# Kernel tuning notes

Hardware: AMD Instinct MI355X
Metric: run time of the kernel (lower is better)

## Reference

```python
import jax, jax.numpy as jnp
import numpy as np

B, S, QD = 4, 2048, 1024
NH, KVH, DH = 16, 4, 64
WIN = 256  # sliding_window


def setup_inputs() -> dict:
    key = jax.random.key(0)
    ks = jax.random.split(key, 5)
    s = QD ** -0.5
    return {
        "hidden_states": jax.random.normal(ks[0], (B, S, QD), jnp.float32),
        "Wq": jax.random.normal(ks[1], (QD, NH * DH), jnp.float32) * s,
        "Wk": jax.random.normal(ks[2], (QD, KVH * DH), jnp.float32) * s,
        "Wv": jax.random.normal(ks[3], (QD, KVH * DH), jnp.float32) * s,
        "Wo": jax.random.normal(ks[4], (NH * DH, QD), jnp.float32) * s,
    }


def reference(hidden_states, Wq, Wk, Wv, Wo):
    x = hidden_states
    # QKV projections (torch Linear, no bias)
    q = (x @ Wq).reshape(B, S, NH, DH).transpose(0, 2, 1, 3)    # [B,NH,S,DH]
    k = (x @ Wk).reshape(B, S, KVH, DH).transpose(0, 2, 1, 3)   # [B,KVH,S,DH]
    v = (x @ Wv).reshape(B, S, KVH, DH).transpose(0, 2, 1, 3)
    # GQA: instead of repeat_interleave on k/v, group query heads per kv head
    g = NH // KVH
    qg = q.reshape(B, KVH, g, S, DH)
    scale = DH ** -0.5
    scores = jnp.einsum('bkgsd,bktd->bkgst', qg, k) * scale      # [B,KVH,g,S,S]
    # Sliding-window mask: torch SDPA treats a FLOAT mask as ADDITIVE, and the
    # original builds a 0/1 float mask (1 where |i-j| <= window). Faithful: add it.
    idx = jnp.arange(S)
    win = (jnp.abs(idx[:, None] - idx[None, :]) <= WIN).astype(scores.dtype)  # [S,S]
    scores = scores + win  # broadcast over B,KVH,g (same mask for all batch/heads)
    attn = jax.nn.softmax(scores, axis=-1)
    out = jnp.einsum('bkgst,bktd->bkgsd', attn, v)               # [B,KVH,g,S,DH]
    out = out.reshape(B, NH, S, DH).transpose(0, 2, 1, 3).reshape(B, S, NH * DH)
    return out @ Wo
```

## Files before the change

### kernel.cpp

```cpp
#include <hip/hip_runtime.h>
#include <hip/hip_bf16.h>


using short8 = __attribute__((ext_vector_type(8))) short;
using f32x4  = __attribute__((ext_vector_type(4))) float;
using f32x16 = __attribute__((ext_vector_type(16))) float;
using uint2v = __attribute__((ext_vector_type(2))) unsigned int;

#define GLDS(g, l) __builtin_amdgcn_global_load_lds( \
    (const __attribute__((address_space(1))) void*)(g), \
    (__attribute__((address_space(3))) void*)(l), 16, 0, 0)

__device__ __forceinline__ unsigned short f2bf(float f) {
  union { float f; unsigned u; } v; v.f = f;
  unsigned r = v.u + 0x7fffu + ((v.u >> 16) & 1u);
  return (unsigned short)(r >> 16);
}

__device__ __forceinline__ unsigned cvtpk(float lo, float hi) {
  unsigned r;
  asm("v_cvt_pk_bf16_f32 %0, %1, %2" : "=v"(r) : "v"(lo), "v"(hi));
  return r;
}

__global__ void cvt_x_kernel(const float* __restrict__ X, unsigned short* __restrict__ Xb) {
  int i = (blockIdx.x * blockDim.x + threadIdx.x) * 4;
  float4 v = *reinterpret_cast<const float4*>(X + i);
  ushort4 o;
  o.x = f2bf(v.x); o.y = f2bf(v.y); o.z = f2bf(v.z); o.w = f2bf(v.w);
  *reinterpret_cast<ushort4*>(Xb + i) = o;
}

__global__ void tr_cvt_kernel(const float* __restrict__ src, unsigned short* __restrict__ dst, int C) {
  int idx = blockIdx.x * blockDim.x + threadIdx.x;
  int c = idx >> 10, r = idx & 1023;
  dst[idx] = f2bf(src[(size_t)r * C + c]);
}

template<int MODE>
__global__ __launch_bounds__(256) void gemm_bt_kernel(
    const unsigned short* __restrict__ A, const unsigned short* __restrict__ Bt,
    unsigned short* __restrict__ Qo, unsigned short* __restrict__ Ko,
    unsigned short* __restrict__ Vto, float* __restrict__ Co)
{
  __shared__ __align__(16) unsigned short As[128 * 32];
  __shared__ __align__(16) unsigned short Bs[128 * 32];
  const int m0 = blockIdx.x * 128;
  const int n0 = blockIdx.y * 128;
  const int t = threadIdx.x;
  const int w = t >> 6, l = t & 63;
  const int wr = w >> 1, wc = w & 1;

  f32x4 acc[4][4] = {};

  const size_t aoff = (size_t)(m0 + w * 16 + (l >> 2)) * 1024 + (size_t)((l & 3) * 8);
  const size_t boff = (size_t)(n0 + w * 16 + (l >> 2)) * 1024 + (size_t)((l & 3) * 8);

  for (int kt = 0; kt < 1024; kt += 32) {
    GLDS(A  + aoff + kt,             &As[w * 512]);
    GLDS(A  + aoff + 64 * 1024 + kt, &As[(w + 4) * 512]);
    GLDS(Bt + boff + kt,             &Bs[w * 512]);
    GLDS(Bt + boff + 64 * 1024 + kt, &Bs[(w + 4) * 512]);
    __syncthreads();

    short8 af[4], bfr[4];
#pragma unroll
    for (int mi = 0; mi < 4; ++mi) {
      int row = wr * 64 + mi * 16 + (l & 15);
      af[mi] = *reinterpret_cast<const short8*>(&As[row * 32 + (l >> 4) * 8]);
    }
#pragma unroll
    for (int ni = 0; ni < 4; ++ni) {
      int row = wc * 64 + ni * 16 + (l & 15);
      bfr[ni] = *reinterpret_cast<const short8*>(&Bs[row * 32 + (l >> 4) * 8]);
    }
#pragma unroll
    for (int mi = 0; mi < 4; ++mi)
#pragma unroll
      for (int ni = 0; ni < 4; ++ni)
        acc[mi][ni] = __builtin_amdgcn_mfma_f32_16x16x32_bf16(af[mi], bfr[ni], acc[mi][ni], 0, 0, 0);
    __syncthreads();
  }

#pragma unroll
  for (int mi = 0; mi < 4; ++mi)
#pragma unroll
    for (int ni = 0; ni < 4; ++ni)
#pragma unroll
      for (int r = 0; r < 4; ++r) {
        int m = m0 + wr * 64 + mi * 16 + (l >> 4) * 4 + r;
        int n = n0 + wc * 64 + ni * 16 + (l & 15);
        float val = acc[mi][ni][r];
        if (MODE == 0) {
          int b = m >> 11, s = m & 2047;
          unsigned short bv = f2bf(val);
          int T = s >> 5;
          if (n < 1024) {
            int h = n >> 6, d = n & 63;
            size_t base = ((((size_t)(b * 16 + h)) * 64 + T) * 4 + (d >> 4)) * 512;
            Qo[base + ((d >> 3) & 1) * 256 + (s & 31) * 8 + (d & 7)] = bv;
          } else if (n < 1280) {
            int kvh = (n - 1024) >> 6, d = n & 63;
            size_t base = ((((size_t)(b * 4 + kvh)) * 64 + T) * 4 + (d >> 4)) * 512;
            Ko[base + ((d >> 3) & 1) * 256 + (s & 31) * 8 + (d & 7)] = bv;
          } else {
            int kvh = (n - 1280) >> 6, d = n & 63;
            size_t base = ((((size_t)(b * 4 + kvh)) * 64 + T) * 4 +
                           ((d >> 5) * 2 + ((s >> 4) & 1))) * 512;
            Vto[base + ((s >> 3) & 1) * 256 + (d & 31) * 8 + (s & 7)] = bv;
          }
        } else {
          Co[((size_t)m << 10) + n] = val;
        }
      }
}

__global__ __launch_bounds__(256, 3) void attn_kernel(
    const unsigned short* __restrict__ Qf, const unsigned short* __restrict__ Kf,
    const unsigned short* __restrict__ Vf, unsigned short* __restrict__ AO)
{
  const int t = threadIdx.x, w = t >> 6, l = t & 63;
  const int hi = l >> 5, ln = l & 31;

  const int orig = blockIdx.x;
  const int swz = (orig & 7) * 128 + (orig >> 3);
  const int hf = swz >> 4;
  const int qt = swz & 15;
  const int b = hf >> 4, h = hf & 15, kvh = h >> 2;
  const int q0 = qt * 128 + w * 32;
  const int qrow = q0 + ln;

  const unsigned short* Qp = Qf + (((size_t)hf * 64 + qt * 4 + w) * 4) * 512;
  const unsigned short* Kp = Kf + ((size_t)(b * 4 + kvh) * 256) * 512;
  const unsigned short* Vp = Vf + ((size_t)(b * 4 + kvh) * 256) * 512;

  short8 qf[4];
#pragma unroll
  for (int kk = 0; kk < 4; ++kk)
    qf[kk] = *reinterpret_cast<const short8*>(Qp + kk * 512 + l * 8);

  f32x16 oA = {}, oB = {};
  float m = -1e30f, lsum = 0.f;
  const float C1  = 0.125f * 1.44269504f;
  const float L2E = 1.44269504f;

  for (int T = 0; T < 64; ++T) {
    const unsigned short* Kt = Kp + (size_t)T * 2048 + l * 8;
    const unsigned short* Vt = Vp + (size_t)T * 2048 + l * 8;
    f32x16 s = {};
#pragma unroll
    for (int kk = 0; kk < 4; ++kk) {
      short8 kfr = *reinterpret_cast<const short8*>(Kt + kk * 512);
      s = __builtin_amdgcn_mfma_f32_32x32x16_bf16(kfr, qf[kk], s, 0, 0, 0);
    }
    short8 vf[4];
#pragma unroll
    for (int j = 0; j < 4; ++j)
      vf[j] = *reinterpret_cast<const short8*>(Vt + j * 512);

    float tv[16];
    const int kv0 = T * 32;
    const int d = q0 - kv0;
    if (d == 256 || d == -256) {
      const int qmb = qrow - kv0 - 4 * hi;
#pragma unroll
      for (int r = 0; r < 16; ++r) {
        const int kc = (r & 3) + 8 * (r >> 2);
        int df = qmb - kc; df = df < 0 ? -df : df;
        tv[r] = s[r] * C1 + (df <= 256 ? L2E : 0.f);
      }
    } else {
      const float addc = (d <= 224 && d >= -224) ? L2E : 0.f;
#pragma unroll
      for (int r = 0; r < 16; ++r)
        tv[r] = s[r] * C1 + addc;
    }

    float t8[8], t4[4], t2[2];
#pragma unroll
    for (int i = 0; i < 8; ++i) t8[i] = fmaxf(tv[i], tv[i + 8]);
#pragma unroll
    for (int i = 0; i < 4; ++i) t4[i] = fmaxf(t8[i], t8[i + 4]);
    t2[0] = fmaxf(t4[0], t4[2]); t2[1] = fmaxf(t4[1], t4[3]);
    float mx = fmaxf(t2[0], t2[1]);
    {
      uint2v sw = __builtin_amdgcn_permlane32_swap(__float_as_uint(mx), __float_as_uint(mx), false, false);
      mx = fmaxf(__uint_as_float(sw[0]), __uint_as_float(sw[1]));
    }
    const float mnew = fmaxf(m, mx);
    if (!__all(mnew - m <= 8.f)) {
      const float f = __builtin_amdgcn_exp2f(m - mnew);
#pragma unroll
      for (int i = 0; i < 16; ++i) { oA[i] *= f; oB[i] *= f; }
      lsum *= f;
      m = mnew;
    }

    float p[16];
#pragma unroll
    for (int i = 0; i < 16; ++i) p[i] = __builtin_amdgcn_exp2f(tv[i] - m);
    float s8[8], s4[4];
#pragma unroll
    for (int i = 0; i < 8; ++i) s8[i] = p[i] + p[i + 8];
#pragma unroll
    for (int i = 0; i < 4; ++i) s4[i] = s8[i] + s8[i + 4];
    float sum = (s4[0] + s4[1]) + (s4[2] + s4[3]);
    {
      uint2v sw = __builtin_amdgcn_permlane32_swap(__float_as_uint(sum), __float_as_uint(sum), false, false);
      sum = __uint_as_float(sw[0]) + __uint_as_float(sw[1]);
    }
    lsum += sum;

#pragma unroll
    for (int ks = 0; ks < 2; ++ks) {
      unsigned a0 = cvtpk(p[ks * 8 + 0], p[ks * 8 + 1]);
      unsigned a1 = cvtpk(p[ks * 8 + 2], p[ks * 8 + 3]);
      unsigned b0 = cvtpk(p[ks * 8 + 4], p[ks * 8 + 5]);
      unsigned b1 = cvtpk(p[ks * 8 + 6], p[ks * 8 + 7]);
      uint2v s0 = __builtin_amdgcn_permlane32_swap(a0, b0, false, false);
      uint2v s1 = __builtin_amdgcn_permlane32_swap(a1, b1, false, false);
      union { unsigned u[4]; short8 v; } pf;
      pf.u[0] = s0[0]; pf.u[1] = s1[0]; pf.u[2] = s0[1]; pf.u[3] = s1[1];
      oA = __builtin_amdgcn_mfma_f32_32x32x16_bf16(vf[ks],     pf.v, oA, 0, 0, 0);
      oB = __builtin_amdgcn_mfma_f32_32x32x16_bf16(vf[2 + ks], pf.v, oB, 0, 0, 0);
    }
  }

  const float inv = 1.f / lsum;
  unsigned short* Op = AO + ((size_t)(b * 2048 + qrow)) * 1024 + h * 64;
#pragma unroll
  for (int qd = 0; qd < 4; ++qd) {
    uint2 wv;
    wv.x = cvtpk(oA[4 * qd + 0] * inv, oA[4 * qd + 1] * inv);
    wv.y = cvtpk(oA[4 * qd + 2] * inv, oA[4 * qd + 3] * inv);
    *reinterpret_cast<uint2*>(Op + qd * 8 + hi * 4) = wv;
  }
#pragma unroll
  for (int qd = 0; qd < 4; ++qd) {
    uint2 wv;
    wv.x = cvtpk(oB[4 * qd + 0] * inv, oB[4 * qd + 1] * inv);
    wv.y = cvtpk(oB[4 * qd + 2] * inv, oB[4 * qd + 3] * inv);
    *reinterpret_cast<uint2*>(Op + 32 + qd * 8 + hi * 4) = wv;
  }
}

extern "C" void kernel_launch(void* const* d_in, const int* in_sizes, int n_in,
                              void* d_out, int out_size, void* d_ws, size_t ws_size,
                              hipStream_t stream)
{
  const float* X  = (const float*)d_in[0];
  const float* Wq = (const float*)d_in[1];
  const float* Wk = (const float*)d_in[2];
  const float* Wv = (const float*)d_in[3];
  const float* Wo = (const float*)d_in[4];
  float* out = (float*)d_out;
  char* ws = (char*)d_ws;

  unsigned short* Xb    = (unsigned short*)(ws);
  unsigned short* WqkvT = (unsigned short*)(ws + 16777216);
  unsigned short* WoT   = (unsigned short*)(ws + 19922944);
  unsigned short* Q     = (unsigned short*)(ws + 22020096);
  unsigned short* Kc    = (unsigned short*)(ws + 38797312);
  unsigned short* Vt    = (unsigned short*)(ws + 42991616);
  unsigned short* AO    = (unsigned short*)(ws + 47185920);

  cvt_x_kernel<<<8192, 256, 0, stream>>>(X, Xb);
  tr_cvt_kernel<<<4096, 256, 0, stream>>>(Wq, WqkvT, 1024);
  tr_cvt_kernel<<<1024, 256, 0, stream>>>(Wk, WqkvT + 1024 * 1024, 256);
  tr_cvt_kernel<<<1024, 256, 0, stream>>>(Wv, WqkvT + 1280 * 1024, 256);
  tr_cvt_kernel<<<4096, 256, 0, stream>>>(Wo, WoT, 1024);

  gemm_bt_kernel<0><<<dim3(64, 12), 256, 0, stream>>>(Xb, WqkvT, Q, Kc, Vt, nullptr);
  attn_kernel<<<1024, 256, 0, stream>>>(Q, Kc, Vt, AO);
  gemm_bt_kernel<1><<<dim3(64, 8), 256, 0, stream>>>(AO, WoT, nullptr, nullptr, nullptr, out);
}
```

Before: 220.4 us.

## Double-buffer K/V fragment loads and fold scaling into exp in unmasked tiles

Restructures the attention loop into a two-stage register ping-pong: the K/V fragments for the next tile are loaded from global memory while the current tile's MFMAs and softmax run, hiding load latency. It also specializes the common non-boundary tile path: the row max is taken on raw scores and the scale plus mask constant is folded into one FMA feeding exp2, which removes a per-element multiply-add pass. The cost is more live vector registers (two sets of K/V fragments) under launch_bounds(256,3), which may cause spills or lower occupancy, plus one redundant load of the last tile.

```diff
diff --git a/kernel.cpp b/kernel.cpp
--- a/kernel.cpp
+++ b/kernel.cpp
@@ -131,8 +131,8 @@
   const int qrow = q0 + ln;
 
   const unsigned short* Qp = Qf + (((size_t)hf * 64 + qt * 4 + w) * 4) * 512;
-  const unsigned short* Kp = Kf + ((size_t)(b * 4 + kvh) * 256) * 512;
-  const unsigned short* Vp = Vf + ((size_t)(b * 4 + kvh) * 256) * 512;
+  const unsigned short* Kp = Kf + ((size_t)(b * 4 + kvh) * 256) * 512 + l * 8;
+  const unsigned short* Vp = Vf + ((size_t)(b * 4 + kvh) * 256) * 512 + l * 8;
 
   short8 qf[4];
 #pragma unroll
@@ -144,24 +144,27 @@
   const float C1  = 0.125f * 1.44269504f;
   const float L2E = 1.44269504f;
 
-  for (int T = 0; T < 64; ++T) {
-    const unsigned short* Kt = Kp + (size_t)T * 2048 + l * 8;
-    const unsigned short* Vt = Vp + (size_t)T * 2048 + l * 8;
+  auto loadfr = [&](short8 (&kf)[4], short8 (&vfr)[4], int T) {
+    const unsigned short* Kt = Kp + (size_t)T * 2048;
+    const unsigned short* Vt = Vp + (size_t)T * 2048;
+#pragma unroll
+    for (int j = 0; j < 4; ++j) {
+      kf[j]  = *reinterpret_cast<const short8*>(Kt + j * 512);
+      vfr[j] = *reinterpret_cast<const short8*>(Vt + j * 512);
+    }
+  };
+
+  auto process = [&](const short8 (&kf)[4], const short8 (&vfr)[4], int T) {
     f32x16 s = {};
 #pragma unroll
-    for (int kk = 0; kk < 4; ++kk) {
-      short8 kfr = *reinterpret_cast<const short8*>(Kt + kk * 512);
-      s = __builtin_amdgcn_mfma_f32_32x32x16_bf16(kfr, qf[kk], s, 0, 0, 0);
-    }
-    short8 vf[4];
-#pragma unroll
-    for (int j = 0; j < 4; ++j)
-      vf[j] = *reinterpret_cast<const short8*>(Vt + j * 512);
-
-    float tv[16];
+    for (int kk = 0; kk < 4; ++kk)
+      s = __builtin_amdgcn_mfma_f32_32x32x16_bf16(kf[kk], qf[kk], s, 0, 0, 0);
+
     const int kv0 = T * 32;
     const int d = q0 - kv0;
+    float p[16];
     if (d == 256 || d == -256) {
+      float tv[16];
       const int qmb = qrow - kv0 - 4 * hi;
 #pragma unroll
       for (int r = 0; r < 16; ++r) {
@@ -169,36 +172,52 @@
         int df = qmb - kc; df = df < 0 ? -df : df;
         tv[r] = s[r] * C1 + (df <= 256 ? L2E : 0.f);
       }
+      float t8[8], t4[4];
+#pragma unroll
+      for (int i = 0; i < 8; ++i) t8[i] = fmaxf(tv[i], tv[i + 8]);
+#pragma unroll
+      for (int i = 0; i < 4; ++i) t4[i] = fmaxf(t8[i], t8[i + 4]);
+      float mx = fmaxf(fmaxf(t4[0], t4[2]), fmaxf(t4[1], t4[3]));
+      {
+        uint2v sw = __builtin_amdgcn_permlane32_swap(__float_as_uint(mx), __float_as_uint(mx), false, false);
+        mx = fmaxf(__uint_as_float(sw[0]), __uint_as_float(sw[1]));
+      }
+      const float mnew = fmaxf(m, mx);
+      if (!__all(mnew - m <= 8.f)) {
+        const float f = __builtin_amdgcn_exp2f(m - mnew);
+#pragma unroll
+        for (int i = 0; i < 16; ++i) { oA[i] *= f; oB[i] *= f; }
+        lsum *= f;
+        m = mnew;
+      }
+#pragma unroll
+      for (int i = 0; i < 16; ++i) p[i] = __builtin_amdgcn_exp2f(tv[i] - m);
     } else {
       const float addc = (d <= 224 && d >= -224) ? L2E : 0.f;
-#pragma unroll
-      for (int r = 0; r < 16; ++r)
-        tv[r] = s[r] * C1 + addc;
-    }
-
-    float t8[8], t4[4], t2[2];
-#pragma unroll
-    for (int i = 0; i < 8; ++i) t8[i] = fmaxf(tv[i], tv[i + 8]);
-#pragma unroll
-    for (int i = 0; i < 4; ++i) t4[i] = fmaxf(t8[i], t8[i + 4]);
-    t2[0] = fmaxf(t4[0], t4[2]); t2[1] = fmaxf(t4[1], t4[3]);
-    float mx = fmaxf(t2[0], t2[1]);
-    {
-      uint2v sw = __builtin_amdgcn_permlane32_swap(__float_as_uint(mx), __float_as_uint(mx), false, false);
-      mx = fmaxf(__uint_as_float(sw[0]), __uint_as_float(sw[1]));
-    }
-    const float mnew = fmaxf(m, mx);
-    if (!__all(mnew - m <= 8.f)) {
-      const float f = __builtin_amdgcn_exp2f(m - mnew);
-#pragma unroll
-      for (int i = 0; i < 16; ++i) { oA[i] *= f; oB[i] *= f; }
-      lsum *= f;
-      m = mnew;
-    }
-
-    float p[16];
-#pragma unroll
-    for (int i = 0; i < 16; ++i) p[i] = __builtin_amdgcn_exp2f(tv[i] - m);
+      float t8[8], t4[4];
+#pragma unroll
+      for (int i = 0; i < 8; ++i) t8[i] = fmaxf(s[i], s[i + 8]);
+#pragma unroll
+      for (int i = 0; i < 4; ++i) t4[i] = fmaxf(t8[i], t8[i + 4]);
+      float mx = fmaxf(fmaxf(t4[0], t4[2]), fmaxf(t4[1], t4[3]));
+      {
+        uint2v sw = __builtin_amdgcn_permlane32_swap(__float_as_uint(mx), __float_as_uint(mx), false, false);
+        mx = fmaxf(__uint_as_float(sw[0]), __uint_as_float(sw[1]));
+      }
+      const float mnew = fmaxf(m, mx * C1 + addc);
+      if (!__all(mnew - m <= 8.f)) {
+        const float f = __builtin_amdgcn_exp2f(m - mnew);
+#pragma unroll
+        for (int i = 0; i < 16; ++i) { oA[i] *= f; oB[i] *= f; }
+        lsum *= f;
+        m = mnew;
+      }
+      const float cc = addc - m;
+#pragma unroll
+      for (int i = 0; i < 16; ++i)
+        p[i] = __builtin_amdgcn_exp2f(__builtin_fmaf(s[i], C1, cc));
+    }
+
     float s8[8], s4[4];
 #pragma unroll
     for (int i = 0; i < 8; ++i) s8[i] = p[i] + p[i + 8];
@@ -221,9 +240,18 @@
       uint2v s1 = __builtin_amdgcn_permlane32_swap(a1, b1, false, false);
       union { unsigned u[4]; short8 v; } pf;
       pf.u[0] = s0[0]; pf.u[1] = s1[0]; pf.u[2] = s0[1]; pf.u[3] = s1[1];
-      oA = __builtin_amdgcn_mfma_f32_32x32x16_bf16(vf[ks],     pf.v, oA, 0, 0, 0);
-      oB = __builtin_amdgcn_mfma_f32_32x32x16_bf16(vf[2 + ks], pf.v, oB, 0, 0, 0);
-    }
+      oA = __builtin_amdgcn_mfma_f32_32x32x16_bf16(vfr[ks],     pf.v, oA, 0, 0, 0);
+      oB = __builtin_amdgcn_mfma_f32_32x32x16_bf16(vfr[2 + ks], pf.v, oB, 0, 0, 0);
+    }
+  };
+
+  short8 kA[4], vA[4], kB[4], vB[4];
+  loadfr(kA, vA, 0);
+  for (int T = 0; T < 64; T += 2) {
+    loadfr(kB, vB, T + 1);
+    process(kA, vA, T);
+    loadfr(kA, vA, T + 2 < 64 ? T + 2 : 63);
+    process(kB, vB, T + 1);
   }
 
   const float inv = 1.f / lsum;
```

Measured after the change: 238.0 us. 1.08x slower.

## Compute softmax row sums via MFMA with ones and trim per-tile VALU work

Applied to the files above, without the earlier changes.

The attention inner loop now accumulates the softmax denominator with an extra MFMA against a ones matrix instead of a VALU add tree plus cross-lane swap. For interior tiles it takes the max on raw scores before scaling and folds scale, mask and max subtraction into a single fma feeding exp2. It also uses 3-input max trees, raises wave priority around the MFMA groups, and advances K/V pointers incrementally. The aim is to cut VALU and permlane work per tile, paid for with one more MFMA per 16-wide k-step and more accumulator registers. Rescaling only lsv[0] relies on every lane holding the same column sums, and the max-before-scale shortcut assumes the positive scale factor.

```diff
diff --git a/kernel.cpp b/kernel.cpp
--- a/kernel.cpp
+++ b/kernel.cpp
@@ -21,6 +21,10 @@
   unsigned r;
   asm("v_cvt_pk_bf16_f32 %0, %1, %2" : "=v"(r) : "v"(lo), "v"(hi));
   return r;
+}
+
+__device__ __forceinline__ float max3f(float a, float b, float c) {
+  return fmaxf(fmaxf(a, b), c);
 }
 
 __global__ void cvt_x_kernel(const float* __restrict__ X, unsigned short* __restrict__ Xb) {
@@ -131,37 +135,45 @@
   const int qrow = q0 + ln;
 
   const unsigned short* Qp = Qf + (((size_t)hf * 64 + qt * 4 + w) * 4) * 512;
-  const unsigned short* Kp = Kf + ((size_t)(b * 4 + kvh) * 256) * 512;
-  const unsigned short* Vp = Vf + ((size_t)(b * 4 + kvh) * 256) * 512;
+  const unsigned short* Kt = Kf + ((size_t)(b * 4 + kvh) * 256) * 512 + l * 8;
+  const unsigned short* Vt = Vf + ((size_t)(b * 4 + kvh) * 256) * 512 + l * 8;
 
   short8 qf[4];
 #pragma unroll
   for (int kk = 0; kk < 4; ++kk)
     qf[kk] = *reinterpret_cast<const short8*>(Qp + kk * 512 + l * 8);
 
-  f32x16 oA = {}, oB = {};
-  float m = -1e30f, lsum = 0.f;
+  const short8 onesf = {(short)0x3F80, (short)0x3F80, (short)0x3F80, (short)0x3F80,
+                        (short)0x3F80, (short)0x3F80, (short)0x3F80, (short)0x3F80};
+  const f32x16 z16 = {};
+
+  f32x16 oA = {}, oB = {}, lsv = {};
+  float m = -1e30f;
   const float C1  = 0.125f * 1.44269504f;
   const float L2E = 1.44269504f;
 
   for (int T = 0; T < 64; ++T) {
-    const unsigned short* Kt = Kp + (size_t)T * 2048 + l * 8;
-    const unsigned short* Vt = Vp + (size_t)T * 2048 + l * 8;
-    f32x16 s = {};
-#pragma unroll
-    for (int kk = 0; kk < 4; ++kk) {
-      short8 kfr = *reinterpret_cast<const short8*>(Kt + kk * 512);
-      s = __builtin_amdgcn_mfma_f32_32x32x16_bf16(kfr, qf[kk], s, 0, 0, 0);
-    }
-    short8 vf[4];
-#pragma unroll
-    for (int j = 0; j < 4; ++j)
-      vf[j] = *reinterpret_cast<const short8*>(Vt + j * 512);
-
-    float tv[16];
+    short8 kf0 = *reinterpret_cast<const short8*>(Kt);
+    short8 kf1 = *reinterpret_cast<const short8*>(Kt + 512);
+    short8 kf2 = *reinterpret_cast<const short8*>(Kt + 1024);
+    short8 kf3 = *reinterpret_cast<const short8*>(Kt + 1536);
+    __builtin_amdgcn_s_setprio(1);
+    f32x16 s = __builtin_amdgcn_mfma_f32_32x32x16_bf16(kf0, qf[0], z16, 0, 0, 0);
+    s = __builtin_amdgcn_mfma_f32_32x32x16_bf16(kf1, qf[1], s, 0, 0, 0);
+    s = __builtin_amdgcn_mfma_f32_32x32x16_bf16(kf2, qf[2], s, 0, 0, 0);
+    s = __builtin_amdgcn_mfma_f32_32x32x16_bf16(kf3, qf[3], s, 0, 0, 0);
+    __builtin_amdgcn_s_setprio(0);
+    short8 vf0 = *reinterpret_cast<const short8*>(Vt);
+    short8 vf1 = *reinterpret_cast<const short8*>(Vt + 512);
+    short8 vf2 = *reinterpret_cast<const short8*>(Vt + 1024);
+    short8 vf3 = *reinterpret_cast<const short8*>(Vt + 1536);
+    Kt += 2048; Vt += 2048;
+
     const int kv0 = T * 32;
     const int d = q0 - kv0;
+    float p[16];
     if (d == 256 || d == -256) {
+      float tv[16];
       const int qmb = qrow - kv0 - 4 * hi;
 #pragma unroll
       for (int r = 0; r < 16; ++r) {
@@ -169,47 +181,51 @@
         int df = qmb - kc; df = df < 0 ? -df : df;
         tv[r] = s[r] * C1 + (df <= 256 ? L2E : 0.f);
       }
+      float a0 = max3f(tv[0], tv[1], tv[2]);
+      float a1 = max3f(tv[3], tv[4], tv[5]);
+      float a2 = max3f(tv[6], tv[7], tv[8]);
+      float a3 = max3f(tv[9], tv[10], tv[11]);
+      float a4 = max3f(tv[12], tv[13], tv[14]);
+      float mx = fmaxf(max3f(a0, a1, a2), max3f(a3, a4, tv[15]));
+      {
+        uint2v sw = __builtin_amdgcn_permlane32_swap(__float_as_uint(mx), __float_as_uint(mx), false, false);
+        mx = fmaxf(__uint_as_float(sw[0]), __uint_as_float(sw[1]));
+      }
+      const float mnew = fmaxf(m, mx);
+      if (!__all(mnew - m <= 8.f)) {
+        const float f = __builtin_amdgcn_exp2f(m - mnew);
+#pragma unroll
+        for (int i = 0; i < 16; ++i) { oA[i] *= f; oB[i] *= f; }
+        lsv[0] *= f;
+        m = mnew;
+      }
+#pragma unroll
+      for (int i = 0; i < 16; ++i) p[i] = __builtin_amdgcn_exp2f(tv[i] - m);
     } else {
       const float addc = (d <= 224 && d >= -224) ? L2E : 0.f;
-#pragma unroll
-      for (int r = 0; r < 16; ++r)
-        tv[r] = s[r] * C1 + addc;
-    }
-
-    float t8[8], t4[4], t2[2];
-#pragma unroll
-    for (int i = 0; i < 8; ++i) t8[i] = fmaxf(tv[i], tv[i + 8]);
-#pragma unroll
-    for (int i = 0; i < 4; ++i) t4[i] = fmaxf(t8[i], t8[i + 4]);
-    t2[0] = fmaxf(t4[0], t4[2]); t2[1] = fmaxf(t4[1], t4[3]);
-    float mx = fmaxf(t2[0], t2[1]);
-    {
-      uint2v sw = __builtin_amdgcn_permlane32_swap(__float_as_uint(mx), __float_as_uint(mx), false, false);
-      mx = fmaxf(__uint_as_float(sw[0]), __uint_as_float(sw[1]));
-    }
-    const float mnew = fmaxf(m, mx);
-    if (!__all(mnew - m <= 8.f)) {
-      const float f = __builtin_amdgcn_exp2f(m - mnew);
-#pragma unroll
-      for (int i = 0; i < 16; ++i) { oA[i] *= f; oB[i] *= f; }
-      lsum *= f;
-      m = mnew;
-    }
-
-    float p[16];
-#pragma unroll
-    for (int i = 0; i < 16; ++i) p[i] = __builtin_amdgcn_exp2f(tv[i] - m);
-    float s8[8], s4[4];
-#pragma unroll
-    for (int i = 0; i < 8; ++i) s8[i] = p[i] + p[i + 8];
-#pragma unroll
-    for (int i = 0; i < 4; ++i) s4[i] = s8[i] + s8[i + 4];
-    float sum = (s4[0] + s4[1]) + (s4[2] + s4[3]);
-    {
-      uint2v sw = __builtin_amdgcn_permlane32_swap(__float_as_uint(sum), __float_as_uint(sum), false, false);
-      sum = __uint_as_float(sw[0]) + __uint_as_float(sw[1]);
-    }
-    lsum += sum;
+      float a0 = max3f(s[0], s[1], s[2]);
+      float a1 = max3f(s[3], s[4], s[5]);
+      float a2 = max3f(s[6], s[7], s[8]);
+      float a3 = max3f(s[9], s[10], s[11]);
+      float a4 = max3f(s[12], s[13], s[14]);
+      float mx = fmaxf(max3f(a0, a1, a2), max3f(a3, a4, s[15]));
+      {
+        uint2v sw = __builtin_amdgcn_permlane32_swap(__float_as_uint(mx), __float_as_uint(mx), false, false);
+        mx = fmaxf(__uint_as_float(sw[0]), __uint_as_float(sw[1]));
+      }
+      const float mnew = fmaxf(m, mx * C1 + addc);
+      if (!__all(mnew - m <= 8.f)) {
+        const float f = __builtin_amdgcn_exp2f(m - mnew);
+#pragma unroll
+        for (int i = 0; i < 16; ++i) { oA[i] *= f; oB[i] *= f; }
+        lsv[0] *= f;
+        m = mnew;
+      }
+      const float cc = addc - m;
+#pragma unroll
+      for (int i = 0; i < 16; ++i)
+        p[i] = __builtin_amdgcn_exp2f(__builtin_fmaf(s[i], C1, cc));
+    }
 
 #pragma unroll
     for (int ks = 0; ks < 2; ++ks) {
@@ -221,12 +237,15 @@
       uint2v s1 = __builtin_amdgcn_permlane32_swap(a1, b1, false, false);
       union { unsigned u[4]; short8 v; } pf;
       pf.u[0] = s0[0]; pf.u[1] = s1[0]; pf.u[2] = s0[1]; pf.u[3] = s1[1];
-      oA = __builtin_amdgcn_mfma_f32_32x32x16_bf16(vf[ks],     pf.v, oA, 0, 0, 0);
-      oB = __builtin_amdgcn_mfma_f32_32x32x16_bf16(vf[2 + ks], pf.v, oB, 0, 0, 0);
-    }
-  }
-
-  const float inv = 1.f / lsum;
+      __builtin_amdgcn_s_setprio(1);
+      oA  = __builtin_amdgcn_mfma_f32_32x32x16_bf16(ks ? vf1 : vf0, pf.v, oA, 0, 0, 0);
+      oB  = __builtin_amdgcn_mfma_f32_32x32x16_bf16(ks ? vf3 : vf2, pf.v, oB, 0, 0, 0);
+      lsv = __builtin_amdgcn_mfma_f32_32x32x16_bf16(onesf,          pf.v, lsv, 0, 0, 0);
+      __builtin_amdgcn_s_setprio(0);
+    }
+  }
+
+  const float inv = 1.f / lsv[0];
   unsigned short* Op = AO + ((size_t)(b * 2048 + qrow)) * 1024 + h * 64;
 #pragma unroll
   for (int qd = 0; qd < 4; ++qd) {
```

Result: slower. 231.0 us (+4.8%).
